# Performance work log

Hardware: AMD Instinct MI355X
Metric: run time of the kernel (lower is better)

Reference implementation:

```python
import jax, jax.numpy as jnp
import numpy as np

B, S, E, H = 4, 2048, 1024, 16
D = E // H  # head_size = 64


def setup_inputs() -> dict:
    key = jax.random.key(0)
    k1, k2 = jax.random.split(key)
    x = jax.random.normal(k1, (B, S, E), dtype=jnp.float32)
    # fused QKV projection weight (torch Linear(E, 3E, bias=False))
    W_qkv = jax.random.normal(k2, (E, 3 * E), dtype=jnp.float32) * (1.0 / np.sqrt(E))
    return {"x": x, "W_qkv": W_qkv}


def reference(x, W_qkv):
    b, s, e = x.shape
    qkv = x @ W_qkv                              # [B,S,3E]
    q, k, v = jnp.split(qkv, 3, axis=-1)
    # [B,S,E] -> [B,H,S,D]
    q = q.reshape(b, s, H, D).transpose(0, 2, 1, 3)
    k = k.reshape(b, s, H, D).transpose(0, 2, 1, 3)
    v = v.reshape(b, s, H, D).transpose(0, 2, 1, 3)
    scores = jnp.einsum("bhqd,bhkd->bhqk", q, k) * (1.0 / np.sqrt(D))
    causal = jnp.tril(jnp.ones((s, s), dtype=bool))  # [S,S]
    scores = jnp.where(causal[None, None, :, :], scores, jnp.float32(-jnp.inf))
    attn = jax.nn.softmax(scores, axis=-1)
    # dropout is identity in eval mode (p effectively 0 for this baseline)
    out = jnp.einsum("bhqk,bhkd->bhqd", attn, v)  # [B,H,S,D]
    out = out.transpose(0, 2, 1, 3).reshape(b, s, e)
    # NOTE: original forward never applies output_projection; faithful omission.
    return out
```

## Files before the change

kernel.cpp:

```cpp
#include <hip/hip_runtime.h>
#include <cstdint>
#include <cstddef>

#define GLOBAL_AS __attribute__((address_space(1)))
#define LDS_AS __attribute__((address_space(3)))

typedef short bf16x8 __attribute__((ext_vector_type(8)));
typedef float f32x4 __attribute__((ext_vector_type(4)));

constexpr int Bq = 4, Sq = 2048, Eq = 1024, Hh = 16;
constexpr int M = Bq * Sq;
constexpr int K = Eq;
constexpr int N = 3 * Eq;

#define SMSC 0.18033688f
#define SMBIAS (-16.0f)

static __device__ __forceinline__ unsigned f2bf(float f) {
    union { float f; unsigned u; } v; v.f = f;
    unsigned r = v.u + 0x7fffu + ((v.u >> 16) & 1u);
    return r >> 16;
}

__global__ __launch_bounds__(256) void cvt_bf16(const float* __restrict__ X,
                                                unsigned short* __restrict__ Xb) {
    size_t i = ((size_t)blockIdx.x * 256 + threadIdx.x) * 8;
    float4 a = *reinterpret_cast<const float4*>(X + i);
    float4 b = *reinterpret_cast<const float4*>(X + i + 4);
    uint4 o;
    o.x = f2bf(a.x) | (f2bf(a.y) << 16);
    o.y = f2bf(a.z) | (f2bf(a.w) << 16);
    o.z = f2bf(b.x) | (f2bf(b.y) << 16);
    o.w = f2bf(b.z) | (f2bf(b.w) << 16);
    *reinterpret_cast<uint4*>(Xb + i) = o;
}

__global__ __launch_bounds__(256) void transpose_w(const float* __restrict__ W,
                                                   unsigned short* __restrict__ Wt) {
    __shared__ unsigned short tile[64 * 72];
    const int t = threadIdx.x;
    const int k0 = blockIdx.y * 64;
    const int n0 = blockIdx.x * 64;
    #pragma unroll
    for (int p = 0; p < 4; ++p) {
        int idx = p * 256 + t;
        int row = idx >> 4;
        int c4 = (idx & 15) * 4;
        float4 v = *reinterpret_cast<const float4*>(W + (size_t)(k0 + row) * N + n0 + c4);
        tile[row * 72 + c4 + 0] = (unsigned short)f2bf(v.x);
        tile[row * 72 + c4 + 1] = (unsigned short)f2bf(v.y);
        tile[row * 72 + c4 + 2] = (unsigned short)f2bf(v.z);
        tile[row * 72 + c4 + 3] = (unsigned short)f2bf(v.w);
    }
    __syncthreads();
    #pragma unroll
    for (int p = 0; p < 2; ++p) {
        int c = t + p * 256;
        int n = c & 63;
        int kc = (c >> 6) * 8;
        unsigned v[8];
        #pragma unroll
        for (int j = 0; j < 8; ++j) v[j] = tile[(kc + j) * 72 + n];
        uint4 o;
        o.x = v[0] | (v[1] << 16);
        o.y = v[2] | (v[3] << 16);
        o.z = v[4] | (v[5] << 16);
        o.w = v[6] | (v[7] << 16);
        *reinterpret_cast<uint4*>(Wt + (size_t)(n0 + n) * K + k0 + kc) = o;
    }
}

__global__ __launch_bounds__(256) void gemm_qkv(const unsigned short* __restrict__ A,
                                                const unsigned short* __restrict__ Bt,
                                                unsigned short* __restrict__ C) {
    __shared__ unsigned short Alds[128 * 64];
    __shared__ unsigned short Blds[128 * 64];
    const int t = threadIdx.x;
    const int lane = t & 63, w = t >> 6;
    const int wm = w >> 1, wn = w & 1;
    const int m0 = blockIdx.y * 128, n0 = blockIdx.x * 128;
    const int lr = lane & 15, quad = lane >> 4;
    const int sw = lr & 7;

    f32x4 acc[4][4] = {};
    for (int k0 = 0; k0 < K; k0 += 64) {
        #pragma unroll
        for (int p = 0; p < 4; ++p) {
            int c = p * 256 + t;
            int row = c >> 3;
            int lch = (c & 7) ^ (row & 7);
            const unsigned short* ga = A + (size_t)(m0 + row) * K + k0 + lch * 8;
            __builtin_amdgcn_global_load_lds((const GLOBAL_AS unsigned int*)ga,
                                             (LDS_AS unsigned int*)&Alds[c * 8], 16, 0, 0);
            const unsigned short* gb = Bt + (size_t)(n0 + row) * K + k0 + lch * 8;
            __builtin_amdgcn_global_load_lds((const GLOBAL_AS unsigned int*)gb,
                                             (LDS_AS unsigned int*)&Blds[c * 8], 16, 0, 0);
        }
        __syncthreads();
        #pragma unroll
        for (int ks = 0; ks < 2; ++ks) {
            bf16x8 af[4], bfr[4];
            const int pch = ((ks * 4 + quad) ^ sw) << 3;
            #pragma unroll
            for (int mt = 0; mt < 4; ++mt)
                af[mt] = *reinterpret_cast<const bf16x8*>(
                    &Alds[(wm * 64 + mt * 16 + lr) * 64 + pch]);
            #pragma unroll
            for (int nt = 0; nt < 4; ++nt)
                bfr[nt] = *reinterpret_cast<const bf16x8*>(
                    &Blds[(wn * 64 + nt * 16 + lr) * 64 + pch]);
            #pragma unroll
            for (int mt = 0; mt < 4; ++mt)
                #pragma unroll
                for (int nt = 0; nt < 4; ++nt)
                    acc[mt][nt] = __builtin_amdgcn_mfma_f32_16x16x32_bf16(af[mt], bfr[nt],
                                                                          acc[mt][nt], 0, 0, 0);
        }
        __syncthreads();
    }
    #pragma unroll
    for (int mt = 0; mt < 4; ++mt)
        #pragma unroll
        for (int nt = 0; nt < 4; ++nt)
            #pragma unroll
            for (int r = 0; r < 4; ++r) {
                int row = m0 + wm * 64 + mt * 16 + quad * 4 + r;
                int col = n0 + wn * 64 + nt * 16 + lr;
                C[(size_t)row * N + col] = (unsigned short)f2bf(acc[mt][nt][r]);
            }
}

__global__ __launch_bounds__(256) void transpose_v(const unsigned short* __restrict__ QKV,
                                                   unsigned short* __restrict__ Vt) {
    __shared__ unsigned short tile[64 * 72];
    const int t = threadIdx.x;
    const int s0 = blockIdx.x * 64;
    const int h = blockIdx.y, b = blockIdx.z;
    #pragma unroll
    for (int p = 0; p < 2; ++p) {
        int c = t + p * 256;
        int row = c >> 3;
        int col0 = (c & 7) * 8;
        *reinterpret_cast<uint4*>(&tile[row * 72 + col0]) =
            *reinterpret_cast<const uint4*>(QKV + (size_t)(b * Sq + s0 + row) * N + 2 * Eq + h * 64 + col0);
    }
    __syncthreads();
    #pragma unroll
    for (int p = 0; p < 2; ++p) {
        int c = t + p * 256;
        int d = c & 63;
        int sc = (c >> 6) * 8;
        unsigned v[8];
        #pragma unroll
        for (int j = 0; j < 8; ++j) v[j] = tile[(sc + j) * 72 + d];
        uint4 o;
        o.x = v[0] | (v[1] << 16);
        o.y = v[2] | (v[3] << 16);
        o.z = v[4] | (v[5] << 16);
        o.w = v[6] | (v[7] << 16);
        *reinterpret_cast<uint4*>(Vt + (size_t)((b * Hh + h) * 64 + d) * Sq + s0 + sc) = o;
    }
}

__global__ __launch_bounds__(256) void flash_attn(const unsigned short* __restrict__ QKV,
                                                  const unsigned short* __restrict__ Vt,
                                                  float* __restrict__ Out) {
    __shared__ unsigned short Klds[2][64 * 64];
    __shared__ unsigned short Vlds[2][64 * 64];
    __shared__ unsigned short Plds[4][32 * 72];
    const int t = threadIdx.x;
    const int lane = t & 63, w = t >> 6;
    const int lr = lane & 15, quad = lane >> 4;
    const int h = blockIdx.y, b = blockIdx.z;
    const unsigned short* Vbase = Vt + (size_t)((b * Hh + h) * 64) * Sq;
    unsigned short* Pl = Plds[w];
    const int sw = lr & 7;

    bf16x8 ones;
    #pragma unroll
    for (int z = 0; z < 8; ++z) ones[z] = (short)0x3F80;

    auto stage = [&](int j, int buf) {
        const int kv0 = j * 64;
        #pragma unroll
        for (int p = 0; p < 2; ++p) {
            int c = p * 256 + t;
            int row = c >> 3;
            int lch = (c & 7) ^ (row & 7);
            const unsigned short* gk = QKV + (size_t)(b * Sq + kv0 + row) * N + Eq + h * 64 + lch * 8;
            __builtin_amdgcn_global_load_lds((const GLOBAL_AS unsigned int*)gk,
                                             (LDS_AS unsigned int*)&Klds[buf][c * 8], 16, 0, 0);
            const unsigned short* gv = Vbase + (size_t)row * Sq + kv0 + lch * 8;
            __builtin_amdgcn_global_load_lds((const GLOBAL_AS unsigned int*)gv,
                                             (LDS_AS unsigned int*)&Vlds[buf][c * 8], 16, 0, 0);
        }
    };

    int qt[2];
    qt[0] = blockIdx.x;
    qt[1] = 15 - blockIdx.x;

    for (int pi = 0; pi < 2; ++pi) {
        const int i = qt[pi];
        const int jmax = 2 * i + 1;
        const int qbase = i * 128 + w * 32;

        bf16x8 qf[2][2];
        #pragma unroll
        for (int mt = 0; mt < 2; ++mt)
            #pragma unroll
            for (int ks = 0; ks < 2; ++ks)
                qf[mt][ks] = *reinterpret_cast<const bf16x8*>(
                    QKV + (size_t)(b * Sq + qbase + mt * 16 + lr) * N + h * 64 + ks * 32 + quad * 8);

        f32x4 o[2][4] = {};
        f32x4 lsum[2] = {};

        __syncthreads();
        stage(0, 0);
        int cur = 0;
        for (int j = 0; j <= jmax; ++j) {
            __syncthreads();
            if (j < jmax) stage(j + 1, cur ^ 1);

            const unsigned short* Kb = Klds[cur];
            const unsigned short* Vb = Vlds[cur];

            f32x4 sa[2][4] = {};
            #pragma unroll
            for (int ks = 0; ks < 2; ++ks) {
                const int pch = ((ks * 4 + quad) ^ sw) << 3;
                #pragma unroll
                for (int nt = 0; nt < 4; ++nt) {
                    bf16x8 kf = *reinterpret_cast<const bf16x8*>(&Kb[(nt * 16 + lr) * 64 + pch]);
                    #pragma unroll
                    for (int mt = 0; mt < 2; ++mt)
                        sa[mt][nt] = __builtin_amdgcn_mfma_f32_16x16x32_bf16(qf[mt][ks], kf,
                                                                             sa[mt][nt], 0, 0, 0);
                }
            }

            const int kv0 = j * 64;
            if (j >= 2 * i) {
                #pragma unroll
                for (int mt = 0; mt < 2; ++mt)
                    #pragma unroll
                    for (int nt = 0; nt < 4; ++nt)
                        #pragma unroll
                        for (int r = 0; r < 4; ++r) {
                            int qg = qbase + mt * 16 + quad * 4 + r;
                            int kvg = kv0 + nt * 16 + lr;
                            float sc = fmaf(sa[mt][nt][r], SMSC, SMBIAS);
                            sc = (kvg > qg) ? -1e30f : sc;
                            Pl[(mt * 16 + quad * 4 + r) * 72 + nt * 16 + lr] =
                                (unsigned short)f2bf(exp2f(sc));
                        }
            } else {
                #pragma unroll
                for (int mt = 0; mt < 2; ++mt)
                    #pragma unroll
                    for (int nt = 0; nt < 4; ++nt)
                        #pragma unroll
                        for (int r = 0; r < 4; ++r)
                            Pl[(mt * 16 + quad * 4 + r) * 72 + nt * 16 + lr] =
                                (unsigned short)f2bf(exp2f(fmaf(sa[mt][nt][r], SMSC, SMBIAS)));
            }
            asm volatile("s_waitcnt lgkmcnt(0)" ::: "memory");

            bf16x8 pf[2][2];
            #pragma unroll
            for (int mt = 0; mt < 2; ++mt)
                #pragma unroll
                for (int ks = 0; ks < 2; ++ks)
                    pf[mt][ks] = *reinterpret_cast<const bf16x8*>(
                        &Pl[(mt * 16 + lr) * 72 + ks * 32 + quad * 8]);

            #pragma unroll
            for (int ks = 0; ks < 2; ++ks) {
                const int pch = ((ks * 4 + quad) ^ sw) << 3;
                #pragma unroll
                for (int dt = 0; dt < 4; ++dt) {
                    bf16x8 vf = *reinterpret_cast<const bf16x8*>(&Vb[(dt * 16 + lr) * 64 + pch]);
                    #pragma unroll
                    for (int mt = 0; mt < 2; ++mt)
                        o[mt][dt] = __builtin_amdgcn_mfma_f32_16x16x32_bf16(pf[mt][ks], vf,
                                                                            o[mt][dt], 0, 0, 0);
                }
                #pragma unroll
                for (int mt = 0; mt < 2; ++mt)
                    lsum[mt] = __builtin_amdgcn_mfma_f32_16x16x32_bf16(pf[mt][ks], ones,
                                                                       lsum[mt], 0, 0, 0);
            }
            cur ^= 1;
        }

        #pragma unroll
        for (int mt = 0; mt < 2; ++mt)
            #pragma unroll
            for (int r = 0; r < 4; ++r) {
                float inv = 1.0f / lsum[mt][r];
                int qg = qbase + mt * 16 + quad * 4 + r;
                #pragma unroll
                for (int dt = 0; dt < 4; ++dt)
                    Out[(size_t)(b * Sq + qg) * Eq + h * 64 + dt * 16 + lr] = o[mt][dt][r] * inv;
            }
    }
}

extern "C" void kernel_launch(void* const* d_in, const int* in_sizes, int n_in,
                              void* d_out, int out_size, void* d_ws, size_t ws_size,
                              hipStream_t stream) {
    const float* x  = (const float*)d_in[0];
    const float* Wq = (const float*)d_in[1];
    float* out = (float*)d_out;

    unsigned short* xb  = (unsigned short*)d_ws;
    unsigned short* qkv = xb + (size_t)M * K;
    unsigned short* Wt  = qkv + (size_t)M * N;
    unsigned short* Vt  = Wt + (size_t)N * K;

    cvt_bf16<<<dim3((M * K) / 2048), 256, 0, stream>>>(x, xb);
    transpose_w<<<dim3(N / 64, K / 64), 256, 0, stream>>>(Wq, Wt);
    gemm_qkv<<<dim3(N / 128, M / 128), 256, 0, stream>>>(xb, Wt, qkv);
    transpose_v<<<dim3(Sq / 64, Hh, Bq), 256, 0, stream>>>(qkv, Vt);
    flash_attn<<<dim3(8, Hh, Bq), 256, 0, stream>>>(qkv, Vt, out);
}
```

Before: 254.6 us.

## Drop LDS staging of K/V in attention, one query tile per block

The attention kernel no longer stages K and V tiles into double-buffered LDS through async global-to-LDS loads and block barriers. Each wave now reads its K and V MFMA fragments straight from global memory (relying on cache), and the probabilities go through an fp32 LDS buffer and are packed to bf16 with the hardware conversion intrinsic. Each block now handles a single query tile instead of a balanced pair, launching twice as many blocks with an occupancy hint. Work per block is now unbalanced, and redundant global/L2 traffic for K/V across the four waves may cost bandwidth. The bf16 conversions in the preprocessing kernels also switch to the packed intrinsic.

```diff
diff --git a/kernel.cpp b/kernel.cpp
--- a/kernel.cpp
+++ b/kernel.cpp
@@ -1,4 +1,5 @@
 #include <hip/hip_runtime.h>
+#include <hip/hip_bf16.h>
 #include <cstdint>
 #include <cstddef>
 
@@ -10,7 +11,7 @@
 
 constexpr int Bq = 4, Sq = 2048, Eq = 1024, Hh = 16;
 constexpr int M = Bq * Sq;
-constexpr int K = Eq;
+constexpr int K = 1024;
 constexpr int N = 3 * Eq;
 
 #define SMSC 0.18033688f
@@ -20,6 +21,12 @@
     union { float f; unsigned u; } v; v.f = f;
     unsigned r = v.u + 0x7fffu + ((v.u >> 16) & 1u);
     return r >> 16;
+}
+
+static __device__ __forceinline__ unsigned pk2(float a, float b) {
+    union { __hip_bfloat162 h; unsigned u; } c;
+    c.h = __float22bfloat162_rn(float2{a, b});
+    return c.u;
 }
 
 __global__ __launch_bounds__(256) void cvt_bf16(const float* __restrict__ X,
@@ -28,10 +35,10 @@
     float4 a = *reinterpret_cast<const float4*>(X + i);
     float4 b = *reinterpret_cast<const float4*>(X + i + 4);
     uint4 o;
-    o.x = f2bf(a.x) | (f2bf(a.y) << 16);
-    o.y = f2bf(a.z) | (f2bf(a.w) << 16);
-    o.z = f2bf(b.x) | (f2bf(b.y) << 16);
-    o.w = f2bf(b.z) | (f2bf(b.w) << 16);
+    o.x = pk2(a.x, a.y);
+    o.y = pk2(a.z, a.w);
+    o.z = pk2(b.x, b.y);
+    o.w = pk2(b.z, b.w);
     *reinterpret_cast<uint4*>(Xb + i) = o;
 }
 
@@ -47,10 +54,8 @@
         int row = idx >> 4;
         int c4 = (idx & 15) * 4;
         float4 v = *reinterpret_cast<const float4*>(W + (size_t)(k0 + row) * N + n0 + c4);
-        tile[row * 72 + c4 + 0] = (unsigned short)f2bf(v.x);
-        tile[row * 72 + c4 + 1] = (unsigned short)f2bf(v.y);
-        tile[row * 72 + c4 + 2] = (unsigned short)f2bf(v.z);
-        tile[row * 72 + c4 + 3] = (unsigned short)f2bf(v.w);
+        *reinterpret_cast<unsigned*>(&tile[row * 72 + c4]) = pk2(v.x, v.y);
+        *reinterpret_cast<unsigned*>(&tile[row * 72 + c4 + 2]) = pk2(v.z, v.w);
     }
     __syncthreads();
     #pragma unroll
@@ -162,149 +167,122 @@
     }
 }
 
-__global__ __launch_bounds__(256) void flash_attn(const unsigned short* __restrict__ QKV,
-                                                  const unsigned short* __restrict__ Vt,
-                                                  float* __restrict__ Out) {
-    __shared__ unsigned short Klds[2][64 * 64];
-    __shared__ unsigned short Vlds[2][64 * 64];
-    __shared__ unsigned short Plds[4][32 * 72];
+__global__ __launch_bounds__(256, 4) void flash_attn(const unsigned short* __restrict__ QKV,
+                                                     const unsigned short* __restrict__ Vt,
+                                                     float* __restrict__ Out) {
+    __shared__ float Plds[4][32 * 68];
     const int t = threadIdx.x;
     const int lane = t & 63, w = t >> 6;
     const int lr = lane & 15, quad = lane >> 4;
     const int h = blockIdx.y, b = blockIdx.z;
+    const int i = 15 - (int)blockIdx.x;
+    const int jmax = 2 * i + 1;
+    const int qbase = i * 128 + w * 32;
+    float* Pl = Plds[w];
+
+    const unsigned short* Kbase = QKV + (size_t)b * Sq * N + Eq + h * 64;
     const unsigned short* Vbase = Vt + (size_t)((b * Hh + h) * 64) * Sq;
-    unsigned short* Pl = Plds[w];
-    const int sw = lr & 7;
 
     bf16x8 ones;
     #pragma unroll
     for (int z = 0; z < 8; ++z) ones[z] = (short)0x3F80;
 
-    auto stage = [&](int j, int buf) {
+    bf16x8 qf[2][2];
+    #pragma unroll
+    for (int mt = 0; mt < 2; ++mt)
+        #pragma unroll
+        for (int ks = 0; ks < 2; ++ks)
+            qf[mt][ks] = *reinterpret_cast<const bf16x8*>(
+                QKV + (size_t)(b * Sq + qbase + mt * 16 + lr) * N + h * 64 + ks * 32 + quad * 8);
+
+    f32x4 o[2][4] = {};
+    f32x4 lsum[2] = {};
+
+    for (int j = 0; j <= jmax; ++j) {
         const int kv0 = j * 64;
-        #pragma unroll
-        for (int p = 0; p < 2; ++p) {
-            int c = p * 256 + t;
-            int row = c >> 3;
-            int lch = (c & 7) ^ (row & 7);
-            const unsigned short* gk = QKV + (size_t)(b * Sq + kv0 + row) * N + Eq + h * 64 + lch * 8;
-            __builtin_amdgcn_global_load_lds((const GLOBAL_AS unsigned int*)gk,
-                                             (LDS_AS unsigned int*)&Klds[buf][c * 8], 16, 0, 0);
-            const unsigned short* gv = Vbase + (size_t)row * Sq + kv0 + lch * 8;
-            __builtin_amdgcn_global_load_lds((const GLOBAL_AS unsigned int*)gv,
-                                             (LDS_AS unsigned int*)&Vlds[buf][c * 8], 16, 0, 0);
-        }
-    };
-
-    int qt[2];
-    qt[0] = blockIdx.x;
-    qt[1] = 15 - blockIdx.x;
-
-    for (int pi = 0; pi < 2; ++pi) {
-        const int i = qt[pi];
-        const int jmax = 2 * i + 1;
-        const int qbase = i * 128 + w * 32;
-
-        bf16x8 qf[2][2];
+
+        f32x4 sa[2][4] = {};
+        #pragma unroll
+        for (int ks = 0; ks < 2; ++ks)
+            #pragma unroll
+            for (int nt = 0; nt < 4; ++nt) {
+                bf16x8 kf = *reinterpret_cast<const bf16x8*>(
+                    Kbase + (size_t)(kv0 + nt * 16 + lr) * N + ks * 32 + quad * 8);
+                #pragma unroll
+                for (int mt = 0; mt < 2; ++mt)
+                    sa[mt][nt] = __builtin_amdgcn_mfma_f32_16x16x32_bf16(qf[mt][ks], kf,
+                                                                         sa[mt][nt], 0, 0, 0);
+            }
+
+        if (j >= 2 * i) {
+            #pragma unroll
+            for (int mt = 0; mt < 2; ++mt)
+                #pragma unroll
+                for (int nt = 0; nt < 4; ++nt)
+                    #pragma unroll
+                    for (int r = 0; r < 4; ++r) {
+                        int qg = qbase + mt * 16 + quad * 4 + r;
+                        int kvg = kv0 + nt * 16 + lr;
+                        float sc = fmaf(sa[mt][nt][r], SMSC, SMBIAS);
+                        sc = (kvg > qg) ? -1e30f : sc;
+                        Pl[(mt * 16 + quad * 4 + r) * 68 + nt * 16 + lr] = exp2f(sc);
+                    }
+        } else {
+            #pragma unroll
+            for (int mt = 0; mt < 2; ++mt)
+                #pragma unroll
+                for (int nt = 0; nt < 4; ++nt)
+                    #pragma unroll
+                    for (int r = 0; r < 4; ++r)
+                        Pl[(mt * 16 + quad * 4 + r) * 68 + nt * 16 + lr] =
+                            exp2f(fmaf(sa[mt][nt][r], SMSC, SMBIAS));
+        }
+        asm volatile("s_waitcnt lgkmcnt(0)" ::: "memory");
+
+        bf16x8 pf[2][2];
         #pragma unroll
         for (int mt = 0; mt < 2; ++mt)
             #pragma unroll
-            for (int ks = 0; ks < 2; ++ks)
-                qf[mt][ks] = *reinterpret_cast<const bf16x8*>(
-                    QKV + (size_t)(b * Sq + qbase + mt * 16 + lr) * N + h * 64 + ks * 32 + quad * 8);
-
-        f32x4 o[2][4] = {};
-        f32x4 lsum[2] = {};
-
-        __syncthreads();
-        stage(0, 0);
-        int cur = 0;
-        for (int j = 0; j <= jmax; ++j) {
-            __syncthreads();
-            if (j < jmax) stage(j + 1, cur ^ 1);
-
-            const unsigned short* Kb = Klds[cur];
-            const unsigned short* Vb = Vlds[cur];
-
-            f32x4 sa[2][4] = {};
-            #pragma unroll
             for (int ks = 0; ks < 2; ++ks) {
-                const int pch = ((ks * 4 + quad) ^ sw) << 3;
-                #pragma unroll
-                for (int nt = 0; nt < 4; ++nt) {
-                    bf16x8 kf = *reinterpret_cast<const bf16x8*>(&Kb[(nt * 16 + lr) * 64 + pch]);
-                    #pragma unroll
-                    for (int mt = 0; mt < 2; ++mt)
-                        sa[mt][nt] = __builtin_amdgcn_mfma_f32_16x16x32_bf16(qf[mt][ks], kf,
-                                                                             sa[mt][nt], 0, 0, 0);
-                }
+                const float* base = &Pl[(mt * 16 + lr) * 68 + ks * 32 + quad * 8];
+                f32x4 lo = *reinterpret_cast<const f32x4*>(base);
+                f32x4 hi = *reinterpret_cast<const f32x4*>(base + 4);
+                union { uint4 u; bf16x8 v; } cv;
+                cv.u.x = pk2(lo[0], lo[1]);
+                cv.u.y = pk2(lo[2], lo[3]);
+                cv.u.z = pk2(hi[0], hi[1]);
+                cv.u.w = pk2(hi[2], hi[3]);
+                pf[mt][ks] = cv.v;
             }
 
-            const int kv0 = j * 64;
-            if (j >= 2 * i) {
+        #pragma unroll
+        for (int ks = 0; ks < 2; ++ks) {
+            #pragma unroll
+            for (int dt = 0; dt < 4; ++dt) {
+                bf16x8 vf = *reinterpret_cast<const bf16x8*>(
+                    Vbase + (size_t)(dt * 16 + lr) * Sq + kv0 + ks * 32 + quad * 8);
                 #pragma unroll
                 for (int mt = 0; mt < 2; ++mt)
-                    #pragma unroll
-                    for (int nt = 0; nt < 4; ++nt)
-                        #pragma unroll
-                        for (int r = 0; r < 4; ++r) {
-                            int qg = qbase + mt * 16 + quad * 4 + r;
-                            int kvg = kv0 + nt * 16 + lr;
-                            float sc = fmaf(sa[mt][nt][r], SMSC, SMBIAS);
-                            sc = (kvg > qg) ? -1e30f : sc;
-                            Pl[(mt * 16 + quad * 4 + r) * 72 + nt * 16 + lr] =
-                                (unsigned short)f2bf(exp2f(sc));
-                        }
-            } else {
-                #pragma unroll
-                for (int mt = 0; mt < 2; ++mt)
-                    #pragma unroll
-                    for (int nt = 0; nt < 4; ++nt)
-                        #pragma unroll
-                        for (int r = 0; r < 4; ++r)
-                            Pl[(mt * 16 + quad * 4 + r) * 72 + nt * 16 + lr] =
-                                (unsigned short)f2bf(exp2f(fmaf(sa[mt][nt][r], SMSC, SMBIAS)));
+                    o[mt][dt] = __builtin_amdgcn_mfma_f32_16x16x32_bf16(pf[mt][ks], vf,
+                                                                        o[mt][dt], 0, 0, 0);
             }
-            asm volatile("s_waitcnt lgkmcnt(0)" ::: "memory");
-
-            bf16x8 pf[2][2];
             #pragma unroll
             for (int mt = 0; mt < 2; ++mt)
-                #pragma unroll
-                for (int ks = 0; ks < 2; ++ks)
-                    pf[mt][ks] = *reinterpret_cast<const bf16x8*>(
-                        &Pl[(mt * 16 + lr) * 72 + ks * 32 + quad * 8]);
-
-            #pragma unroll
-            for (int ks = 0; ks < 2; ++ks) {
-                const int pch = ((ks * 4 + quad) ^ sw) << 3;
-                #pragma unroll
-                for (int dt = 0; dt < 4; ++dt) {
-                    bf16x8 vf = *reinterpret_cast<const bf16x8*>(&Vb[(dt * 16 + lr) * 64 + pch]);
-                    #pragma unroll
-                    for (int mt = 0; mt < 2; ++mt)
-                        o[mt][dt] = __builtin_amdgcn_mfma_f32_16x16x32_bf16(pf[mt][ks], vf,
-                                                                            o[mt][dt], 0, 0, 0);
-                }
-                #pragma unroll
-                for (int mt = 0; mt < 2; ++mt)
-                    lsum[mt] = __builtin_amdgcn_mfma_f32_16x16x32_bf16(pf[mt][ks], ones,
-                                                                       lsum[mt], 0, 0, 0);
-            }
-            cur ^= 1;
-        }
-
-        #pragma unroll
-        for (int mt = 0; mt < 2; ++mt)
-            #pragma unroll
-            for (int r = 0; r < 4; ++r) {
-                float inv = 1.0f / lsum[mt][r];
-                int qg = qbase + mt * 16 + quad * 4 + r;
-                #pragma unroll
-                for (int dt = 0; dt < 4; ++dt)
-                    Out[(size_t)(b * Sq + qg) * Eq + h * 64 + dt * 16 + lr] = o[mt][dt][r] * inv;
-            }
-    }
+                lsum[mt] = __builtin_amdgcn_mfma_f32_16x16x32_bf16(pf[mt][ks], ones,
+                                                                   lsum[mt], 0, 0, 0);
+        }
+    }
+
+    #pragma unroll
+    for (int mt = 0; mt < 2; ++mt)
+        #pragma unroll
+        for (int r = 0; r < 4; ++r) {
+            float inv = 1.0f / lsum[mt][r];
+            int qg = qbase + mt * 16 + quad * 4 + r;
+            #pragma unroll
+            for (int dt = 0; dt < 4; ++dt)
+                Out[(size_t)(b * Sq + qg) * Eq + h * 64 + dt * 16 + lr] = o[mt][dt][r] * inv;
+        }
 }
 
 extern "C" void kernel_launch(void* const* d_in, const int* in_sizes, int n_in,
@@ -323,5 +301,5 @@
     transpose_w<<<dim3(N / 64, K / 64), 256, 0, stream>>>(Wq, Wt);
     gemm_qkv<<<dim3(N / 128, M / 128), 256, 0, stream>>>(xb, Wt, qkv);
     transpose_v<<<dim3(Sq / 64, Hh, Bq), 256, 0, stream>>>(qkv, Vt);
-    flash_attn<<<dim3(8, Hh, Bq), 256, 0, stream>>>(qkv, Vt, out);
-}
+    flash_attn<<<dim3(16, Hh, Bq), 256, 0, stream>>>(qkv, Vt, out);
+}
```

New measurement: 430.8 us. 69.2% more time.

## Merge prep kernels, give each query tile its own attention block, skip masked tiles

Applied to the files above, without the earlier changes.

The x conversion and W transpose kernels become a single launch, and float-to-bf16 packing now uses the hardware __float22bfloat162_rn intrinsic. Flash attention previously handled a paired short and long query tile in one block. It now launches one block per query tile, longest tiles first, so there are twice as many smaller blocks. Each wave also skips the final KV tile when that tile is fully masked for its rows, while still joining the staging barriers. The P values are truncated to bf16 instead of rounded, trading a little precision for fewer instructions.

```diff
diff --git a/kernel.cpp b/kernel.cpp
--- a/kernel.cpp
+++ b/kernel.cpp
@@ -1,4 +1,5 @@
 #include <hip/hip_runtime.h>
+#include <hip/hip_bf16.h>
 #include <cstdint>
 #include <cstddef>
 
@@ -10,7 +11,7 @@
 
 constexpr int Bq = 4, Sq = 2048, Eq = 1024, Hh = 16;
 constexpr int M = Bq * Sq;
-constexpr int K = Eq;
+constexpr int K = 1024;
 constexpr int N = 3 * Eq;
 
 #define SMSC 0.18033688f
@@ -22,35 +23,42 @@
     return r >> 16;
 }
 
-__global__ __launch_bounds__(256) void cvt_bf16(const float* __restrict__ X,
-                                                unsigned short* __restrict__ Xb) {
-    size_t i = ((size_t)blockIdx.x * 256 + threadIdx.x) * 8;
-    float4 a = *reinterpret_cast<const float4*>(X + i);
-    float4 b = *reinterpret_cast<const float4*>(X + i + 4);
-    uint4 o;
-    o.x = f2bf(a.x) | (f2bf(a.y) << 16);
-    o.y = f2bf(a.z) | (f2bf(a.w) << 16);
-    o.z = f2bf(b.x) | (f2bf(b.y) << 16);
-    o.w = f2bf(b.z) | (f2bf(b.w) << 16);
-    *reinterpret_cast<uint4*>(Xb + i) = o;
-}
-
-__global__ __launch_bounds__(256) void transpose_w(const float* __restrict__ W,
-                                                   unsigned short* __restrict__ Wt) {
+static __device__ __forceinline__ unsigned pk2(float a, float b) {
+    union { __hip_bfloat162 h; unsigned u; } c;
+    c.h = __float22bfloat162_rn(float2{a, b});
+    return c.u;
+}
+
+__global__ __launch_bounds__(256) void prep(const float* __restrict__ X,
+                                            unsigned short* __restrict__ Xb,
+                                            const float* __restrict__ W,
+                                            unsigned short* __restrict__ Wt) {
     __shared__ unsigned short tile[64 * 72];
     const int t = threadIdx.x;
-    const int k0 = blockIdx.y * 64;
-    const int n0 = blockIdx.x * 64;
+    const int bx = blockIdx.x;
+    if (bx < 4096) {
+        size_t i = ((size_t)bx * 256 + t) * 8;
+        float4 a = *reinterpret_cast<const float4*>(X + i);
+        float4 b = *reinterpret_cast<const float4*>(X + i + 4);
+        uint4 o;
+        o.x = pk2(a.x, a.y);
+        o.y = pk2(a.z, a.w);
+        o.z = pk2(b.x, b.y);
+        o.w = pk2(b.z, b.w);
+        *reinterpret_cast<uint4*>(Xb + i) = o;
+        return;
+    }
+    const int idx = bx - 4096;
+    const int n0 = (idx % 48) * 64;
+    const int k0 = (idx / 48) * 64;
     #pragma unroll
     for (int p = 0; p < 4; ++p) {
-        int idx = p * 256 + t;
-        int row = idx >> 4;
-        int c4 = (idx & 15) * 4;
+        int c = p * 256 + t;
+        int row = c >> 4;
+        int c4 = (c & 15) * 4;
         float4 v = *reinterpret_cast<const float4*>(W + (size_t)(k0 + row) * N + n0 + c4);
-        tile[row * 72 + c4 + 0] = (unsigned short)f2bf(v.x);
-        tile[row * 72 + c4 + 1] = (unsigned short)f2bf(v.y);
-        tile[row * 72 + c4 + 2] = (unsigned short)f2bf(v.z);
-        tile[row * 72 + c4 + 3] = (unsigned short)f2bf(v.w);
+        *reinterpret_cast<unsigned*>(&tile[row * 72 + c4]) = pk2(v.x, v.y);
+        *reinterpret_cast<unsigned*>(&tile[row * 72 + c4 + 2]) = pk2(v.z, v.w);
     }
     __syncthreads();
     #pragma unroll
@@ -171,10 +179,17 @@
     const int t = threadIdx.x;
     const int lane = t & 63, w = t >> 6;
     const int lr = lane & 15, quad = lane >> 4;
-    const int h = blockIdx.y, b = blockIdx.z;
-    const unsigned short* Vbase = Vt + (size_t)((b * Hh + h) * 64) * Sq;
+    const int hb = blockIdx.x;
+    const int h = hb & 15, b = hb >> 4;
+    const int i = 15 - (int)blockIdx.y;
+    const int jmax = 2 * i + 1;
+    const int jd = 2 * i + (w >> 1);
+    const int qbase = i * 128 + w * 32;
     unsigned short* Pl = Plds[w];
     const int sw = lr & 7;
+
+    const unsigned short* Kbase = QKV + (size_t)b * Sq * N + Eq + h * 64;
+    const unsigned short* Vbase = Vt + (size_t)((b * Hh + h) * 64) * Sq;
 
     bf16x8 ones;
     #pragma unroll
@@ -187,7 +202,7 @@
             int c = p * 256 + t;
             int row = c >> 3;
             int lch = (c & 7) ^ (row & 7);
-            const unsigned short* gk = QKV + (size_t)(b * Sq + kv0 + row) * N + Eq + h * 64 + lch * 8;
+            const unsigned short* gk = Kbase + (size_t)(kv0 + row) * N + lch * 8;
             __builtin_amdgcn_global_load_lds((const GLOBAL_AS unsigned int*)gk,
                                              (LDS_AS unsigned int*)&Klds[buf][c * 8], 16, 0, 0);
             const unsigned short* gv = Vbase + (size_t)row * Sq + kv0 + lch * 8;
@@ -196,35 +211,27 @@
         }
     };
 
-    int qt[2];
-    qt[0] = blockIdx.x;
-    qt[1] = 15 - blockIdx.x;
-
-    for (int pi = 0; pi < 2; ++pi) {
-        const int i = qt[pi];
-        const int jmax = 2 * i + 1;
-        const int qbase = i * 128 + w * 32;
-
-        bf16x8 qf[2][2];
-        #pragma unroll
-        for (int mt = 0; mt < 2; ++mt)
-            #pragma unroll
-            for (int ks = 0; ks < 2; ++ks)
-                qf[mt][ks] = *reinterpret_cast<const bf16x8*>(
-                    QKV + (size_t)(b * Sq + qbase + mt * 16 + lr) * N + h * 64 + ks * 32 + quad * 8);
-
-        f32x4 o[2][4] = {};
-        f32x4 lsum[2] = {};
-
+    bf16x8 qf[2][2];
+    #pragma unroll
+    for (int mt = 0; mt < 2; ++mt)
+        #pragma unroll
+        for (int ks = 0; ks < 2; ++ks)
+            qf[mt][ks] = *reinterpret_cast<const bf16x8*>(
+                QKV + (size_t)(b * Sq + qbase + mt * 16 + lr) * N + h * 64 + ks * 32 + quad * 8);
+
+    f32x4 o[2][4] = {};
+    f32x4 lsum[2] = {};
+
+    stage(0, 0);
+    int cur = 0;
+    for (int j = 0; j <= jmax; ++j) {
         __syncthreads();
-        stage(0, 0);
-        int cur = 0;
-        for (int j = 0; j <= jmax; ++j) {
-            __syncthreads();
-            if (j < jmax) stage(j + 1, cur ^ 1);
-
+        if (j < jmax) stage(j + 1, cur ^ 1);
+
+        if (j <= jd) {
             const unsigned short* Kb = Klds[cur];
             const unsigned short* Vb = Vlds[cur];
+            const int kv0 = j * 64;
 
             f32x4 sa[2][4] = {};
             #pragma unroll
@@ -240,8 +247,7 @@
                 }
             }
 
-            const int kv0 = j * 64;
-            if (j >= 2 * i) {
+            if (j == jd) {
                 #pragma unroll
                 for (int mt = 0; mt < 2; ++mt)
                     #pragma unroll
@@ -253,7 +259,7 @@
                             float sc = fmaf(sa[mt][nt][r], SMSC, SMBIAS);
                             sc = (kvg > qg) ? -1e30f : sc;
                             Pl[(mt * 16 + quad * 4 + r) * 72 + nt * 16 + lr] =
-                                (unsigned short)f2bf(exp2f(sc));
+                                (unsigned short)(__float_as_uint(exp2f(sc)) >> 16);
                         }
             } else {
                 #pragma unroll
@@ -263,7 +269,8 @@
                         #pragma unroll
                         for (int r = 0; r < 4; ++r)
                             Pl[(mt * 16 + quad * 4 + r) * 72 + nt * 16 + lr] =
-                                (unsigned short)f2bf(exp2f(fmaf(sa[mt][nt][r], SMSC, SMBIAS)));
+                                (unsigned short)(__float_as_uint(
+                                    exp2f(fmaf(sa[mt][nt][r], SMSC, SMBIAS))) >> 16);
             }
             asm volatile("s_waitcnt lgkmcnt(0)" ::: "memory");
 
@@ -291,20 +298,20 @@
                     lsum[mt] = __builtin_amdgcn_mfma_f32_16x16x32_bf16(pf[mt][ks], ones,
                                                                        lsum[mt], 0, 0, 0);
             }
-            cur ^= 1;
-        }
-
-        #pragma unroll
-        for (int mt = 0; mt < 2; ++mt)
-            #pragma unroll
-            for (int r = 0; r < 4; ++r) {
-                float inv = 1.0f / lsum[mt][r];
-                int qg = qbase + mt * 16 + quad * 4 + r;
-                #pragma unroll
-                for (int dt = 0; dt < 4; ++dt)
-                    Out[(size_t)(b * Sq + qg) * Eq + h * 64 + dt * 16 + lr] = o[mt][dt][r] * inv;
-            }
-    }
+        }
+        cur ^= 1;
+    }
+
+    #pragma unroll
+    for (int mt = 0; mt < 2; ++mt)
+        #pragma unroll
+        for (int r = 0; r < 4; ++r) {
+            float inv = 1.0f / lsum[mt][r];
+            int qg = qbase + mt * 16 + quad * 4 + r;
+            #pragma unroll
+            for (int dt = 0; dt < 4; ++dt)
+                Out[(size_t)(b * Sq + qg) * Eq + h * 64 + dt * 16 + lr] = o[mt][dt][r] * inv;
+        }
 }
 
 extern "C" void kernel_launch(void* const* d_in, const int* in_sizes, int n_in,
@@ -319,9 +326,8 @@
     unsigned short* Wt  = qkv + (size_t)M * N;
     unsigned short* Vt  = Wt + (size_t)N * K;
 
-    cvt_bf16<<<dim3((M * K) / 2048), 256, 0, stream>>>(x, xb);
-    transpose_w<<<dim3(N / 64, K / 64), 256, 0, stream>>>(Wq, Wt);
+    prep<<<dim3(4096 + 768), 256, 0, stream>>>(x, xb, Wq, Wt);
     gemm_qkv<<<dim3(N / 128, M / 128), 256, 0, stream>>>(xb, Wt, qkv);
     transpose_v<<<dim3(Sq / 64, Hh, Bq), 256, 0, stream>>>(qkv, Vt);
-    flash_attn<<<dim3(8, Hh, Bq), 256, 0, stream>>>(qkv, Vt, out);
-}
+    flash_attn<<<dim3(Hh * Bq, 16), 256, 0, stream>>>(qkv, Vt, out);
+}
```

New measurement: 249.1 us. 1.02x faster.
